# Kernel optimization log

Measured on AMD Instinct MI355X. Metric: run time of the kernel, lower is better.

## Reference

```python
import jax, jax.numpy as jnp
import numpy as np

H = 1024        # hidden_dim
NH = 8          # num_heads
HD = H // NH    # head_dim
EPS = 1e-5


def setup_inputs() -> dict:
    key = jax.random.key(0)
    ks = jax.random.split(key, 16)
    s = 0.02
    d = {
        'x': jax.random.normal(ks[0], (2, 2048, H), dtype=jnp.float32),
        'ln1_g': jnp.ones((H,), jnp.float32), 'ln1_b': jnp.zeros((H,), jnp.float32),
        'ln2_g': jnp.ones((H,), jnp.float32), 'ln2_b': jnp.zeros((H,), jnp.float32),
        'Wq': jax.random.normal(ks[1], (H, H), jnp.float32) * s,
        'bq': jnp.zeros((H,), jnp.float32),
        'Wk': jax.random.normal(ks[2], (H, H), jnp.float32) * s,
        'bk': jnp.zeros((H,), jnp.float32),
        'Wv': jax.random.normal(ks[3], (H, H), jnp.float32) * s,
        'bv': jnp.zeros((H,), jnp.float32),
        'Wo': jax.random.normal(ks[4], (H, H), jnp.float32) * s,
        'bo': jnp.zeros((H,), jnp.float32),
        'W1': jax.random.normal(ks[5], (H, 4 * H), jnp.float32) * s,
        'b1': jnp.zeros((4 * H,), jnp.float32),
        'W2': jax.random.normal(ks[6], (4 * H, H), jnp.float32) * s,
        'b2': jnp.zeros((H,), jnp.float32),
    }
    return d


def _layernorm(x, g, b):
    mu = jnp.mean(x, axis=-1, keepdims=True)
    var = jnp.mean(jnp.square(x - mu), axis=-1, keepdims=True)
    return (x - mu) * jax.lax.rsqrt(var + EPS) * g + b


def _block(x, ln1_g, ln1_b, ln2_g, ln2_b, Wq, bq, Wk, bk, Wv, bv, Wo, bo, W1, b1, W2, b2):
    B, S, _ = x.shape
    h = _layernorm(x, ln1_g, ln1_b)
    q = (h @ Wq + bq).reshape(B, S, NH, HD).transpose(0, 2, 1, 3)  # [B,NH,S,HD]
    k = (h @ Wk + bk).reshape(B, S, NH, HD).transpose(0, 2, 1, 3)
    v = (h @ Wv + bv).reshape(B, S, NH, HD).transpose(0, 2, 1, 3)
    scores = jnp.einsum('bhqd,bhkd->bhqk', q, k) / np.sqrt(HD)
    causal = jnp.tril(jnp.ones((S, S), bool))
    scores = jnp.where(causal, scores, -jnp.inf)
    attn = jax.nn.softmax(scores, axis=-1)
    y = jnp.einsum('bhqk,bhkd->bhqd', attn, v).transpose(0, 2, 1, 3).reshape(B, S, H)
    x = x + y @ Wo + bo
    h2 = _layernorm(x, ln2_g, ln2_b)
    m = jax.nn.gelu(h2 @ W1 + b1, approximate=False) @ W2 + b2
    return x + m


def reference(x, ln1_g, ln1_b, ln2_g, ln2_b, Wq, bq, Wk, bk, Wv, bv, Wo, bo, W1, b1, W2, b2):
    return _block(x, ln1_g, ln1_b, ln2_g, ln2_b, Wq, bq, Wk, bk, Wv, bv, Wo, bo, W1, b1, W2, b2)
```

## Files before the change

kernel.cpp:

```cpp
#include <hip/hip_runtime.h>
#include <hip/hip_bf16.h>
#include <math.h>

using bf16 = __hip_bfloat16;
typedef __attribute__((ext_vector_type(8))) short short8v;
typedef __attribute__((ext_vector_type(4))) float f32x4;

#define DEV __device__ __forceinline__

DEV void load_lds16(const bf16* gsrc, bf16* ldst) {
  __builtin_amdgcn_global_load_lds((const __attribute__((address_space(1))) void*)gsrc,
                                   (__attribute__((address_space(3))) void*)ldst, 16, 0, 0);
}

DEV void swz8(int& bx, int& by, int gx, int gy) {
  const int n = gx * gy, c = n >> 3;
  int lin = bx + gx * by;
  lin = (lin & 7) * c + (lin >> 3);
  bx = lin % gx; by = lin / gx;
}

DEV unsigned pack2bf(float a, float b) {
  bf16 ba = __float2bfloat16(a), bb = __float2bfloat16(b);
  return (unsigned)*(unsigned short*)&ba | ((unsigned)*(unsigned short*)&bb << 16);
}

__global__ __launch_bounds__(256) void prep_kernel(
    const float* __restrict__ Wq, const float* __restrict__ Wk, const float* __restrict__ Wv,
    const float* __restrict__ Wo, const float* __restrict__ W1, const float* __restrict__ W2,
    bf16* __restrict__ WqT, bf16* __restrict__ WkT, bf16* __restrict__ WvT,
    bf16* __restrict__ WoT, bf16* __restrict__ W1T, bf16* __restrict__ W2T,
    const float* __restrict__ x, const float* __restrict__ ln1g, const float* __restrict__ ln1b,
    bf16* __restrict__ h) {
  __shared__ float tile[64][65];
  const int b = blockIdx.x;
  if (b >= 3072) {
    const int row = b - 3072, t = threadIdx.x;
    const float4 v = ((const float4*)(x + (size_t)row * 1024))[t];
    float s = v.x + v.y + v.z + v.w;
#pragma unroll
    for (int mm = 1; mm < 64; mm <<= 1) s += __shfl_xor(s, mm);
    __shared__ float r1[4], r2[4];
    if ((t & 63) == 0) r1[t >> 6] = s;
    __syncthreads();
    const float mean = (r1[0] + r1[1] + r1[2] + r1[3]) * (1.0f / 1024.0f);
    const float d0 = v.x - mean, d1 = v.y - mean, d2 = v.z - mean, d3 = v.w - mean;
    float s2 = d0 * d0 + d1 * d1 + d2 * d2 + d3 * d3;
#pragma unroll
    for (int mm = 1; mm < 64; mm <<= 1) s2 += __shfl_xor(s2, mm);
    if ((t & 63) == 0) r2[t >> 6] = s2;
    __syncthreads();
    const float var = (r2[0] + r2[1] + r2[2] + r2[3]) * (1.0f / 1024.0f);
    const float rinv = rsqrtf(var + 1e-5f);
    const int c = t * 4;
    bf16* o = h + (size_t)row * 1024 + c;
    o[0] = __float2bfloat16(d0 * rinv * ln1g[c + 0] + ln1b[c + 0]);
    o[1] = __float2bfloat16(d1 * rinv * ln1g[c + 1] + ln1b[c + 1]);
    o[2] = __float2bfloat16(d2 * rinv * ln1g[c + 2] + ln1b[c + 2]);
    o[3] = __float2bfloat16(d3 * rinv * ln1g[c + 3] + ln1b[c + 3]);
    return;
  }
  const float* W; bf16* WT; int K, N, n0, k0;
  if (b < 1024) {
    const int which = b >> 8, t = b & 255;
    W  = (which == 0) ? Wq  : (which == 1) ? Wk  : (which == 2) ? Wv  : Wo;
    WT = (which == 0) ? WqT : (which == 1) ? WkT : (which == 2) ? WvT : WoT;
    K = 1024; N = 1024; n0 = (t & 15) * 64; k0 = (t >> 4) * 64;
  } else if (b < 2048) {
    const int t = b - 1024;
    W = W1; WT = W1T; K = 1024; N = 4096; n0 = (t & 63) * 64; k0 = (t >> 6) * 64;
  } else {
    const int t = b - 2048;
    W = W2; WT = W2T; K = 4096; N = 1024; n0 = (t & 15) * 64; k0 = (t >> 4) * 64;
  }
  const int tx = threadIdx.x & 15, ty = threadIdx.x >> 4;
#pragma unroll
  for (int p = 0; p < 4; ++p) {
    int r = p * 16 + ty;
    float4 vv = *(const float4*)&W[(size_t)(k0 + r) * N + n0 + tx * 4];
    tile[r][tx * 4 + 0] = vv.x; tile[r][tx * 4 + 1] = vv.y;
    tile[r][tx * 4 + 2] = vv.z; tile[r][tx * 4 + 3] = vv.w;
  }
  __syncthreads();
#pragma unroll
  for (int p = 0; p < 4; ++p) {
    int n = p * 16 + ty;
    bf16* dst = WT + (size_t)(n0 + n) * K + k0 + tx * 4;
#pragma unroll
    for (int j = 0; j < 4; ++j) dst[j] = __float2bfloat16(tile[tx * 4 + j][n]);
  }
}

__global__ __launch_bounds__(256) void ln_kernel(const float* __restrict__ x,
                                                 const float* __restrict__ g,
                                                 const float* __restrict__ b,
                                                 bf16* __restrict__ out) {
  const int row = blockIdx.x, t = threadIdx.x;
  const float4 v = ((const float4*)(x + (size_t)row * 1024))[t];
  float s = v.x + v.y + v.z + v.w;
#pragma unroll
  for (int mm = 1; mm < 64; mm <<= 1) s += __shfl_xor(s, mm);
  __shared__ float r1[4], r2[4];
  if ((t & 63) == 0) r1[t >> 6] = s;
  __syncthreads();
  const float mean = (r1[0] + r1[1] + r1[2] + r1[3]) * (1.0f / 1024.0f);
  const float d0 = v.x - mean, d1 = v.y - mean, d2 = v.z - mean, d3 = v.w - mean;
  float s2 = d0 * d0 + d1 * d1 + d2 * d2 + d3 * d3;
#pragma unroll
  for (int mm = 1; mm < 64; mm <<= 1) s2 += __shfl_xor(s2, mm);
  if ((t & 63) == 0) r2[t >> 6] = s2;
  __syncthreads();
  const float var = (r2[0] + r2[1] + r2[2] + r2[3]) * (1.0f / 1024.0f);
  const float rinv = rsqrtf(var + 1e-5f);
  const int c = t * 4;
  bf16* o = out + (size_t)row * 1024 + c;
  o[0] = __float2bfloat16(d0 * rinv * g[c + 0] + b[c + 0]);
  o[1] = __float2bfloat16(d1 * rinv * g[c + 1] + b[c + 1]);
  o[2] = __float2bfloat16(d2 * rinv * g[c + 2] + b[c + 2]);
  o[3] = __float2bfloat16(d3 * rinv * g[c + 3] + b[c + 3]);
}

template <int EPI>
__global__ __launch_bounds__(512, 2) void gemm256(
    const bf16* __restrict__ A, const bf16* __restrict__ BT,
    const float* __restrict__ bias0, const float* __restrict__ bias1, const float* __restrict__ bias2,
    void* __restrict__ outp, int M, int N, int K) {
  __shared__ bf16 As[4][256 * 32];
  __shared__ bf16 Bs[4][256 * 32];
  const int tid = threadIdx.x;
  const int w = tid >> 6, l = tid & 63;
  const int wm = w >> 2, wn = w & 3;
  const int c = l & 15, h4 = l >> 4;
  int bx = blockIdx.x, by = blockIdx.y;
  swz8(bx, by, gridDim.x, gridDim.y);
  const int m0 = by * 256, n0 = bx * 256;

  const float* bias;
  int zz = 0;
  if (EPI == 0) {
    zz = n0 >> 10;
    bias = ((zz == 0) ? bias0 : (zz == 1) ? bias1 : bias2) - (zz << 10);
  } else {
    bias = bias0;
  }

  const int rl = l >> 2;
  const int ch = (l & 3) * 8;
  const int nkt = K >> 5;

  f32x4 acc[8][4] = {};

  auto STAGE_A = [&](int t, int b) {
    const bf16* src = A + (size_t)(m0 + rl) * K + t * 32 + ch;
    load_lds16(src + (size_t)((w * 2 + 0) * 16) * K, &As[b][(w * 2 + 0) * 512]);
    load_lds16(src + (size_t)((w * 2 + 1) * 16) * K, &As[b][(w * 2 + 1) * 512]);
  };
  auto STAGE_B = [&](int t, int b) {
    const bf16* src = BT + (size_t)(n0 + rl) * K + t * 32 + ch;
    load_lds16(src + (size_t)((w * 2 + 0) * 16) * K, &Bs[b][(w * 2 + 0) * 512]);
    load_lds16(src + (size_t)((w * 2 + 1) * 16) * K, &Bs[b][(w * 2 + 1) * 512]);
  };

  STAGE_A(0, 0); STAGE_B(0, 0);
  STAGE_A(1, 1); STAGE_B(1, 1);
  STAGE_A(2, 2); STAGE_B(2, 2);
  asm volatile("s_waitcnt vmcnt(8)" ::: "memory");
  __builtin_amdgcn_sched_barrier(0);
  __builtin_amdgcn_s_barrier();

  for (int t = 0; t < nkt; ++t) {
    const bf16* Ab = &As[t & 3][0];
    const bf16* Bb = &Bs[t & 3][0];
    short8v a[4], b[4];
#pragma unroll
    for (int i = 0; i < 4; ++i)
      a[i] = *(const short8v*)&Ab[(wm * 128 + i * 16 + c) * 32 + h4 * 8];
#pragma unroll
    for (int i = 0; i < 4; ++i)
      b[i] = *(const short8v*)&Bb[(wn * 64 + i * 16 + c) * 32 + h4 * 8];
    if (t + 3 < nkt) STAGE_A(t + 3, (t + 3) & 3);
    asm volatile("s_waitcnt lgkmcnt(0)" ::: "memory");
    __builtin_amdgcn_sched_barrier(0);
    __builtin_amdgcn_s_setprio(1);
#pragma unroll
    for (int mi = 0; mi < 4; ++mi)
#pragma unroll
      for (int ni = 0; ni < 4; ++ni)
        acc[mi][ni] = __builtin_amdgcn_mfma_f32_16x16x32_bf16(a[mi], b[ni], acc[mi][ni], 0, 0, 0);
    __builtin_amdgcn_s_setprio(0);
#pragma unroll
    for (int i = 0; i < 4; ++i)
      a[i] = *(const short8v*)&Ab[(wm * 128 + 64 + i * 16 + c) * 32 + h4 * 8];
    if (t + 3 < nkt) STAGE_B(t + 3, (t + 3) & 3);
    asm volatile("s_waitcnt lgkmcnt(0)" ::: "memory");
    __builtin_amdgcn_sched_barrier(0);
    __builtin_amdgcn_s_setprio(1);
#pragma unroll
    for (int mi = 0; mi < 4; ++mi)
#pragma unroll
      for (int ni = 0; ni < 4; ++ni)
        acc[4 + mi][ni] = __builtin_amdgcn_mfma_f32_16x16x32_bf16(a[mi], b[ni], acc[4 + mi][ni], 0, 0, 0);
    __builtin_amdgcn_s_setprio(0);
    if (t < nkt - 3)       asm volatile("s_waitcnt vmcnt(8)" ::: "memory");
    else if (t == nkt - 3) asm volatile("s_waitcnt vmcnt(4)" ::: "memory");
    else                   asm volatile("s_waitcnt vmcnt(0)" ::: "memory");
    __builtin_amdgcn_sched_barrier(0);
    __builtin_amdgcn_s_barrier();
  }

#pragma unroll
  for (int mi = 0; mi < 8; ++mi) {
#pragma unroll
    for (int ni = 0; ni < 4; ++ni) {
#pragma unroll
      for (int r = 0; r < 4; ++r) {
        const int m = m0 + wm * 128 + mi * 16 + h4 * 4 + r;
        const int n = n0 + wn * 64 + ni * 16 + c;
        const float vv = acc[mi][ni][r] + bias[n];
        if (EPI == 0) {
          const int bb = m >> 11, ss = m & 2047;
          const int n1 = n - (zz << 10);
          const int hh = n1 >> 7, dd = n1 & 127;
          ((bf16*)outp)[(size_t)zz * 4194304 + (((size_t)bb * 8 + hh) * 2048 + ss) * 128 + dd] =
              __float2bfloat16(vv);
        } else {
          const size_t idx = (size_t)m * N + n;
          const float u = 0.7978845608028654f * (vv + 0.044715f * vv * vv * vv);
          const float tt = __expf(2.0f * u);
          const float th = 1.0f - 2.0f / (tt + 1.0f);
          ((bf16*)outp)[idx] = __float2bfloat16(0.5f * vv * (1.0f + th));
        }
      }
    }
  }
}

template <int EPI, int MI>
__global__ __launch_bounds__(256) void gemm128(
    const bf16* __restrict__ A, const bf16* __restrict__ BT,
    const float* __restrict__ bias0, const float* __restrict__ bias1, const float* __restrict__ bias2,
    const float* __restrict__ res, void* __restrict__ outp,
    int M, int N, int K) {
  __shared__ bf16 As[2][MI * 1024];
  __shared__ bf16 Bs[2][128 * 32];
  const int tid = threadIdx.x;
  const int w = tid >> 6, l = tid & 63;
  const int wr = w >> 1, wc = w & 1;
  const int col = l & 15, hi = l >> 4;
  int bx = blockIdx.x, by = blockIdx.y;
  swz8(bx, by, gridDim.x, gridDim.y);
  const int m0 = by * (32 * MI), n0 = bx * 128;

  const float* bias = bias0;

  const int srow = l >> 2;
  const int scol = ((l & 3) ^ ((l >> 4) & 3)) * 8;
  const int rs = col * 4 + (hi ^ ((l >> 2) & 3));
  f32x4 acc[MI][4] = {};

  const int nk = K >> 5;
#pragma unroll
  for (int j = 0; j < MI / 2; ++j) {
    const int grp = w * (MI / 2) + j;
    load_lds16(A + (size_t)(m0 + grp * 16 + srow) * K + scol, &As[0][grp * 512]);
  }
#pragma unroll
  for (int j = 0; j < 2; ++j) {
    const int grp = w * 2 + j;
    load_lds16(BT + (size_t)(n0 + grp * 16 + srow) * K + scol, &Bs[0][grp * 512]);
  }
  __syncthreads();

  int cur = 0;
  for (int kt = 0; kt < nk; ++kt) {
    if (kt + 1 < nk) {
      const int k0n = (kt + 1) * 32;
#pragma unroll
      for (int j = 0; j < MI / 2; ++j) {
        const int grp = w * (MI / 2) + j;
        load_lds16(A + (size_t)(m0 + grp * 16 + srow) * K + k0n + scol, &As[cur ^ 1][grp * 512]);
      }
#pragma unroll
      for (int j = 0; j < 2; ++j) {
        const int grp = w * 2 + j;
        load_lds16(BT + (size_t)(n0 + grp * 16 + srow) * K + k0n + scol, &Bs[cur ^ 1][grp * 512]);
      }
    }
    __builtin_amdgcn_sched_barrier(0);

    short8v af[MI], bfr[4];
#pragma unroll
    for (int i = 0; i < MI; ++i)
      af[i] = *(const short8v*)&As[cur][(wr * MI + i) * 512 + rs * 8];
#pragma unroll
    for (int i = 0; i < 4; ++i)
      bfr[i] = *(const short8v*)&Bs[cur][(wc * 4 + i) * 512 + rs * 8];
#pragma unroll
    for (int mi = 0; mi < MI; ++mi)
#pragma unroll
      for (int ni = 0; ni < 4; ++ni)
        acc[mi][ni] = __builtin_amdgcn_mfma_f32_16x16x32_bf16(af[mi], bfr[ni], acc[mi][ni], 0, 0, 0);
    __syncthreads();
    cur ^= 1;
  }

#pragma unroll
  for (int mi = 0; mi < MI; ++mi) {
#pragma unroll
    for (int ni = 0; ni < 4; ++ni) {
#pragma unroll
      for (int r = 0; r < 4; ++r) {
        const int m = m0 + wr * (16 * MI) + mi * 16 + hi * 4 + r;
        const int n = n0 + wc * 64 + ni * 16 + col;
        const float vv = acc[mi][ni][r] + bias[n];
        const size_t idx = (size_t)m * N + n;
        ((float*)outp)[idx] = res[idx] + vv;
      }
    }
  }
}

__global__ __launch_bounds__(512, 1) void gemm_sk2(
    const bf16* __restrict__ A, const bf16* __restrict__ BT,
    const float* __restrict__ bias, const float* __restrict__ res, float* __restrict__ outp,
    int M, int N, int K) {
  __shared__ __align__(16) char lds_raw[131072];
  const int tid = threadIdx.x;
  const int w = tid >> 6, l = tid & 63;
  const int grp = w >> 2, wg = w & 3;
  const int wr = wg >> 1, wc = wg & 1;
  const int col = l & 15, hi = l >> 4;
  int bx = blockIdx.x, by = blockIdx.y;
  swz8(bx, by, gridDim.x, gridDim.y);
  const int m0 = by * 128, n0 = bx * 128;

  const int rl = l >> 2;
  const int ch = (l & 3) * 8;
  f32x4 acc[4][4] = {};

  const int KH = K >> 1;
  const int kbase = grp * KH;
  const int nkt = KH >> 5;

  auto ABUF = [&](int b) { return (bf16*)(lds_raw + grp * 65536 + b * 16384); };
  auto BBUF = [&](int b) { return (bf16*)(lds_raw + grp * 65536 + b * 16384 + 8192); };

  auto STAGE = [&](int t, int b) {
    const bf16* srcA = A + (size_t)(m0 + rl) * K + kbase + t * 32 + ch;
    const bf16* srcB = BT + (size_t)(n0 + rl) * K + kbase + t * 32 + ch;
    bf16* Ab = ABUF(b); bf16* Bb = BBUF(b);
    load_lds16(srcA + (size_t)((wg * 2 + 0) * 16) * K, Ab + (wg * 2 + 0) * 512);
    load_lds16(srcA + (size_t)((wg * 2 + 1) * 16) * K, Ab + (wg * 2 + 1) * 512);
    load_lds16(srcB + (size_t)((wg * 2 + 0) * 16) * K, Bb + (wg * 2 + 0) * 512);
    load_lds16(srcB + (size_t)((wg * 2 + 1) * 16) * K, Bb + (wg * 2 + 1) * 512);
  };

  STAGE(0, 0); STAGE(1, 1); STAGE(2, 2);
  asm volatile("s_waitcnt vmcnt(8)" ::: "memory");
  __builtin_amdgcn_sched_barrier(0);
  __builtin_amdgcn_s_barrier();

  for (int t = 0; t < nkt; ++t) {
    const bf16* Ab = ABUF(t & 3);
    const bf16* Bb = BBUF(t & 3);
    short8v af[4], bf_[4];
#pragma unroll
    for (int i = 0; i < 4; ++i) {
      af[i]  = *(const short8v*)&Ab[(wr * 64 + i * 16 + col) * 32 + hi * 8];
      bf_[i] = *(const short8v*)&Bb[(wc * 64 + i * 16 + col) * 32 + hi * 8];
    }
    if (t + 3 < nkt) STAGE(t + 3, (t + 3) & 3);
    asm volatile("s_waitcnt lgkmcnt(0)" ::: "memory");
    __builtin_amdgcn_sched_barrier(0);
    __builtin_amdgcn_s_setprio(1);
#pragma unroll
    for (int mi = 0; mi < 4; ++mi)
#pragma unroll
      for (int ni = 0; ni < 4; ++ni)
        acc[mi][ni] = __builtin_amdgcn_mfma_f32_16x16x32_bf16(af[mi], bf_[ni], acc[mi][ni], 0, 0, 0);
    __builtin_amdgcn_s_setprio(0);
    if (t < nkt - 3)       asm volatile("s_waitcnt vmcnt(8)" ::: "memory");
    else if (t == nkt - 3) asm volatile("s_waitcnt vmcnt(4)" ::: "memory");
    else                   asm volatile("s_waitcnt vmcnt(0)" ::: "memory");
    __builtin_amdgcn_sched_barrier(0);
    __builtin_amdgcn_s_barrier();
  }

  float* dump = (float*)lds_raw;
  if (grp == 1) {
#pragma unroll
    for (int mi = 0; mi < 4; ++mi)
#pragma unroll
      for (int ni = 0; ni < 4; ++ni)
#pragma unroll
        for (int r = 0; r < 4; ++r)
          dump[(wr * 64 + mi * 16 + hi * 4 + r) * 130 + wc * 64 + ni * 16 + col] = acc[mi][ni][r];
  }
  __syncthreads();
  if (grp == 0) {
#pragma unroll
    for (int mi = 0; mi < 4; ++mi) {
#pragma unroll
      for (int ni = 0; ni < 4; ++ni) {
#pragma unroll
        for (int r = 0; r < 4; ++r) {
          const int lrow = wr * 64 + mi * 16 + hi * 4 + r;
          const int lcol = wc * 64 + ni * 16 + col;
          const int m = m0 + lrow, n = n0 + lcol;
          const size_t idx = (size_t)m * N + n;
          outp[idx] = res[idx] + acc[mi][ni][r] + dump[lrow * 130 + lcol] + bias[n];
        }
      }
    }
  }
}

__global__ __launch_bounds__(512) void attn_kernel(const bf16* __restrict__ q,
                                                   const bf16* __restrict__ k,
                                                   const bf16* __restrict__ v,
                                                   bf16* __restrict__ y) {
  __shared__ __align__(16) char lds_raw[157696];
  int p = blockIdx.x, bh = blockIdx.y;
  swz8(p, bh, 16, 16);
  const int tid = threadIdx.x;
  const int w = tid >> 6, l = tid & 63;
  const int grp = w >> 2, wg = w & 3;
  const int col = l & 15, hi = l >> 4;

  const bf16* kbase = k + (size_t)bh * 2048 * 128;
  const bf16* vbase = v + (size_t)bh * 2048 * 128;
  const int bb = bh >> 3, hh = bh & 7;

  bf16* Psw = (bf16*)(lds_raw + 139264 + (size_t)w * 2304);

  const int klr = (l >> 4);
  const int kblk0 = l & 15;
  const int vr = (l & 31) * 2;
  const int vcb = (wg * 2 + (l >> 5)) * 16;

  const float scale = 0.08838834764831845f;

  for (int half = 0; half < 2; ++half) {
    const int qt = half ? p : (31 - p);
    const int q0 = qt * 64;
    const int T = qt + 1;
    const int n0 = (T + 1) >> 1;
    const int myn = grp ? (T >> 1) : n0;
    const int tb = grp ? n0 : 0;

    short8v qf[4];
    const bf16* qp = q + ((size_t)bh * 2048 + q0 + wg * 16 + col) * 128;
#pragma unroll
    for (int c = 0; c < 4; ++c) qf[c] = *(const short8v*)(qp + c * 32 + hi * 8);

    f32x4 o[8] = {};
    float mx = -1e30f, sm = 0.f;

    if (myn > 0) {
      bf16* Ks0 = (bf16*)(lds_raw + (size_t)(grp * 2 + 0) * 16384);
      bf16* Vt0 = (bf16*)(lds_raw + 65536 + (size_t)(grp * 2 + 0) * 18432);
#pragma unroll
      for (int j = 0; j < 4; ++j) {
        const int lr = j * 4 + klr;
        const int blk = kblk0 ^ (lr & 7);
        load_lds16(kbase + (size_t)(tb * 64 + wg * 16 + lr) * 128 + blk * 8,
                   Ks0 + wg * 2048 + j * 512);
      }
      const bf16* vsrc = vbase + (size_t)(tb * 64 + vr) * 128 + vcb;
      short8v v00 = *(const short8v*)vsrc;
      short8v v01 = *(const short8v*)(vsrc + 8);
      short8v v10 = *(const short8v*)(vsrc + 128);
      short8v v11 = *(const short8v*)(vsrc + 136);
#pragma unroll
      for (int i = 0; i < 8; ++i) {
        *(unsigned int*)&Vt0[(vcb + i) * 72 + vr] =
            ((unsigned int)(unsigned short)v00[i]) | (((unsigned int)(unsigned short)v10[i]) << 16);
        *(unsigned int*)&Vt0[(vcb + 8 + i) * 72 + vr] =
            ((unsigned int)(unsigned short)v01[i]) | (((unsigned int)(unsigned short)v11[i]) << 16);
      }
    }
    __syncthreads();

    for (int it = 0; it < n0; ++it) {
      const int cur = it & 1;
      const bool active = it < myn;
      const bool havenext = (it + 1) < myn;
      bf16* KsCur = (bf16*)(lds_raw + (size_t)(grp * 2 + cur) * 16384);
      bf16* KsNxt = (bf16*)(lds_raw + (size_t)(grp * 2 + (cur ^ 1)) * 16384);
      bf16* VtCur = (bf16*)(lds_raw + 65536 + (size_t)(grp * 2 + cur) * 18432);
      bf16* VtNxt = (bf16*)(lds_raw + 65536 + (size_t)(grp * 2 + (cur ^ 1)) * 18432);

      short8v v00, v01, v10, v11;
      if (havenext) {
        const int nt = tb + it + 1;
#pragma unroll
        for (int j = 0; j < 4; ++j) {
          const int lr = j * 4 + klr;
          const int blk = kblk0 ^ (lr & 7);
          load_lds16(kbase + (size_t)(nt * 64 + wg * 16 + lr) * 128 + blk * 8,
                     KsNxt + wg * 2048 + j * 512);
        }
        const bf16* vsrc = vbase + (size_t)(nt * 64 + vr) * 128 + vcb;
        v00 = *(const short8v*)vsrc;
        v01 = *(const short8v*)(vsrc + 8);
        v10 = *(const short8v*)(vsrc + 128);
        v11 = *(const short8v*)(vsrc + 136);
      }

      if (active) {
        const int ktile = tb + it;
        f32x4 s[4] = {};
        __builtin_amdgcn_s_setprio(1);
#pragma unroll
        for (int c4 = 0; c4 < 4; ++c4) {
#pragma unroll
          for (int kg = 0; kg < 4; ++kg) {
            const int kr = kg * 16 + col;
            short8v kf = *(const short8v*)&KsCur[kr * 128 + ((c4 * 32 + hi * 8) ^ ((col & 7) << 3))];
            s[kg] = __builtin_amdgcn_mfma_f32_16x16x32_bf16(kf, qf[c4], s[kg], 0, 0, 0);
          }
        }
        __builtin_amdgcn_s_setprio(0);

        const bool diag = (ktile == qt);
        const int qloc = wg * 16 + col;
#pragma unroll
        for (int kg = 0; kg < 4; ++kg) {
#pragma unroll
          for (int r = 0; r < 4; ++r) {
            float a = s[kg][r] * scale;
            if (diag && (kg * 16 + hi * 4 + r > qloc)) a = -1e30f;
            s[kg][r] = a;
          }
        }
        f32x4 m4;
#pragma unroll
        for (int r = 0; r < 4; ++r)
          m4[r] = fmaxf(fmaxf(s[0][r], s[1][r]), fmaxf(s[2][r], s[3][r]));
        float t = fmaxf(fmaxf(m4[0], m4[1]), fmaxf(m4[2], m4[3]));
        t = fmaxf(t, __shfl_xor(t, 16));
        t = fmaxf(t, __shfl_xor(t, 32));
        const float mn = fmaxf(mx, t);
        const float aa = __expf(mx - mn);
        float ps = 0.f;
        unsigned pk0[4], pk1[4];
#pragma unroll
        for (int kg = 0; kg < 4; ++kg) {
          const float p0 = __expf(s[kg][0] - mn);
          const float p1 = __expf(s[kg][1] - mn);
          const float p2 = __expf(s[kg][2] - mn);
          const float p3 = __expf(s[kg][3] - mn);
          ps += (p0 + p1) + (p2 + p3);
          pk0[kg] = pack2bf(p0, p1);
          pk1[kg] = pack2bf(p2, p3);
        }
        ps += __shfl_xor(ps, 16);
        ps += __shfl_xor(ps, 32);
        sm = sm * aa + ps;
        mx = mn;
#pragma unroll
        for (int kg = 0; kg < 4; ++kg) {
          *(unsigned*)&Psw[col * 72 + kg * 16 + hi * 4]     = pk0[kg];
          *(unsigned*)&Psw[col * 72 + kg * 16 + hi * 4 + 2] = pk1[kg];
        }
#pragma unroll
        for (int db = 0; db < 8; ++db) {
          o[db][0] *= aa; o[db][1] *= aa; o[db][2] *= aa; o[db][3] *= aa;
        }
      }

      if (havenext) {
#pragma unroll
        for (int i = 0; i < 8; ++i) {
          *(unsigned int*)&VtNxt[(vcb + i) * 72 + vr] =
              ((unsigned int)(unsigned short)v00[i]) | (((unsigned int)(unsigned short)v10[i]) << 16);
          *(unsigned int*)&VtNxt[(vcb + 8 + i) * 72 + vr] =
              ((unsigned int)(unsigned short)v01[i]) | (((unsigned int)(unsigned short)v11[i]) << 16);
        }
      }

      if (active) {
        asm volatile("s_waitcnt lgkmcnt(0)" ::: "memory");
        __builtin_amdgcn_s_setprio(1);
#pragma unroll
        for (int ks = 0; ks < 2; ++ks) {
          short8v pf = *(const short8v*)&Psw[col * 72 + ks * 32 + hi * 8];
#pragma unroll
          for (int db = 0; db < 8; ++db) {
            short8v vf = *(const short8v*)&VtCur[(db * 16 + col) * 72 + ks * 32 + hi * 8];
            o[db] = __builtin_amdgcn_mfma_f32_16x16x32_bf16(vf, pf, o[db], 0, 0, 0);
          }
        }
        __builtin_amdgcn_s_setprio(0);
      }
      __syncthreads();
    }

    if (grp == 1) {
      float* Mo = (float*)(lds_raw + (size_t)wg * 8448);
      float* Ml = (float*)(lds_raw + 33792 + (size_t)wg * 128);
#pragma unroll
      for (int db = 0; db < 8; ++db)
        *(f32x4*)&Mo[col * 132 + db * 16 + hi * 4] = o[db];
      if (hi == 0) { Ml[col * 2] = mx; Ml[col * 2 + 1] = sm; }
    }
    __syncthreads();
    if (grp == 0) {
      const float* Mo = (const float*)(lds_raw + (size_t)wg * 8448);
      const float* Ml = (const float*)(lds_raw + 33792 + (size_t)wg * 128);
      const float m1 = Ml[col * 2], l1 = Ml[col * 2 + 1];
      const float M = fmaxf(mx, m1);
      const float a0 = __expf(mx - M);
      const float a1 = __expf(m1 - M);
      const float inv = 1.0f / (sm * a0 + l1 * a1);
      const int qg = q0 + wg * 16 + col;
      bf16* yrow = y + ((size_t)bb * 2048 + qg) * 1024 + hh * 128;
#pragma unroll
      for (int db = 0; db < 8; ++db) {
        f32x4 rd = *(const f32x4*)&Mo[col * 132 + db * 16 + hi * 4];
        const unsigned w0 = pack2bf((o[db][0] * a0 + rd[0] * a1) * inv,
                                    (o[db][1] * a0 + rd[1] * a1) * inv);
        const unsigned w1 = pack2bf((o[db][2] * a0 + rd[2] * a1) * inv,
                                    (o[db][3] * a0 + rd[3] * a1) * inv);
        uint2 pk; pk.x = w0; pk.y = w1;
        *(uint2*)(yrow + db * 16 + hi * 4) = pk;
      }
    }
    __syncthreads();
  }
}

extern "C" void kernel_launch(void* const* d_in, const int* in_sizes, int n_in,
                              void* d_out, int out_size, void* d_ws, size_t ws_size,
                              hipStream_t stream) {
  const float* x    = (const float*)d_in[0];
  const float* ln1g = (const float*)d_in[1];
  const float* ln1b = (const float*)d_in[2];
  const float* ln2g = (const float*)d_in[3];
  const float* ln2b = (const float*)d_in[4];
  const float* Wq   = (const float*)d_in[5];
  const float* bq   = (const float*)d_in[6];
  const float* Wk   = (const float*)d_in[7];
  const float* bk   = (const float*)d_in[8];
  const float* Wv   = (const float*)d_in[9];
  const float* bv   = (const float*)d_in[10];
  const float* Wo   = (const float*)d_in[11];
  const float* bo   = (const float*)d_in[12];
  const float* W1   = (const float*)d_in[13];
  const float* b1   = (const float*)d_in[14];
  const float* W2   = (const float*)d_in[15];
  const float* b2   = (const float*)d_in[16];
  float* out = (float*)d_out;
  char* ws = (char*)d_ws;
  const size_t MB = 1024 * 1024;

  bf16* WqT = (bf16*)(ws + 0 * MB);
  bf16* WkT = (bf16*)(ws + 2 * MB);
  bf16* WvT = (bf16*)(ws + 4 * MB);
  bf16* WoT = (bf16*)(ws + 6 * MB);
  bf16* W1T = (bf16*)(ws + 8 * MB);
  bf16* W2T = (bf16*)(ws + 16 * MB);
  bf16* h   = (bf16*)(ws + 24 * MB);
  bf16* qb  = (bf16*)(ws + 32 * MB);
  bf16* kb  = (bf16*)(ws + 40 * MB);
  bf16* vb  = (bf16*)(ws + 48 * MB);
  bf16* y   = (bf16*)(ws + 56 * MB);
  bf16* g   = (bf16*)(ws + 32 * MB);
  float* x1 = (float*)(ws + 64 * MB);
  bf16* h2  = h;

  prep_kernel<<<7168, 256, 0, stream>>>(Wq, Wk, Wv, Wo, W1, W2, WqT, WkT, WvT, WoT, W1T, W2T,
                                        x, ln1g, ln1b, h);

  gemm256<0><<<dim3(12, 16), 512, 0, stream>>>(h, WqT, bq, bk, bv, qb, 4096, 3072, 1024);

  attn_kernel<<<dim3(16, 16), 512, 0, stream>>>(qb, kb, vb, y);

  gemm128<1, 2><<<dim3(8, 64), 256, 0, stream>>>(y, WoT, bo, nullptr, nullptr, x, x1,
                                                 4096, 1024, 1024);

  ln_kernel<<<4096, 256, 0, stream>>>(x1, ln2g, ln2b, h2);

  gemm256<2><<<dim3(16, 16), 512, 0, stream>>>(h2, W1T, b1, nullptr, nullptr, g,
                                               4096, 4096, 1024);

  gemm_sk2<<<dim3(8, 32), 512, 0, stream>>>(g, W2T, b2, x1, out, 4096, 1024, 4096);
}
```

Baseline: 220.9 us.

## Fold softmax scale into Q projection, lazy rescale, reuse split-K GEMM for Wo

The 1/sqrt(HD) attention scale is now applied to Q in the QKV GEMM epilogue, so the per-score multiply in the attention loop goes away and causal masking runs only on diagonal tiles. The online softmax skips the running-max update and output rescale when every lane's new tile max stays within 8 of the current max, which saves exp and multiply work on most tiles. The Wo projection drops the 128-tile gemm128 kernel and uses the existing gemm_sk2 split-K kernel with residual add. The lazy max update lets exp values reach about e^8 before a rescale, which is fine for fp32 but could cost some bf16 precision in P.

```diff
diff --git a/kernel.cpp b/kernel.cpp
--- a/kernel.cpp
+++ b/kernel.cpp
@@ -216,8 +216,9 @@
       for (int r = 0; r < 4; ++r) {
         const int m = m0 + wm * 128 + mi * 16 + h4 * 4 + r;
         const int n = n0 + wn * 64 + ni * 16 + c;
-        const float vv = acc[mi][ni][r] + bias[n];
+        float vv = acc[mi][ni][r] + bias[n];
         if (EPI == 0) {
+          if (zz == 0) vv *= 0.08838834764831845f;
           const int bb = m >> 11, ss = m & 2047;
           const int n1 = n - (zz << 10);
           const int hh = n1 >> 7, dd = n1 & 127;
@@ -230,91 +231,6 @@
           const float th = 1.0f - 2.0f / (tt + 1.0f);
           ((bf16*)outp)[idx] = __float2bfloat16(0.5f * vv * (1.0f + th));
         }
-      }
-    }
-  }
-}
-
-template <int EPI, int MI>
-__global__ __launch_bounds__(256) void gemm128(
-    const bf16* __restrict__ A, const bf16* __restrict__ BT,
-    const float* __restrict__ bias0, const float* __restrict__ bias1, const float* __restrict__ bias2,
-    const float* __restrict__ res, void* __restrict__ outp,
-    int M, int N, int K) {
-  __shared__ bf16 As[2][MI * 1024];
-  __shared__ bf16 Bs[2][128 * 32];
-  const int tid = threadIdx.x;
-  const int w = tid >> 6, l = tid & 63;
-  const int wr = w >> 1, wc = w & 1;
-  const int col = l & 15, hi = l >> 4;
-  int bx = blockIdx.x, by = blockIdx.y;
-  swz8(bx, by, gridDim.x, gridDim.y);
-  const int m0 = by * (32 * MI), n0 = bx * 128;
-
-  const float* bias = bias0;
-
-  const int srow = l >> 2;
-  const int scol = ((l & 3) ^ ((l >> 4) & 3)) * 8;
-  const int rs = col * 4 + (hi ^ ((l >> 2) & 3));
-  f32x4 acc[MI][4] = {};
-
-  const int nk = K >> 5;
-#pragma unroll
-  for (int j = 0; j < MI / 2; ++j) {
-    const int grp = w * (MI / 2) + j;
-    load_lds16(A + (size_t)(m0 + grp * 16 + srow) * K + scol, &As[0][grp * 512]);
-  }
-#pragma unroll
-  for (int j = 0; j < 2; ++j) {
-    const int grp = w * 2 + j;
-    load_lds16(BT + (size_t)(n0 + grp * 16 + srow) * K + scol, &Bs[0][grp * 512]);
-  }
-  __syncthreads();
-
-  int cur = 0;
-  for (int kt = 0; kt < nk; ++kt) {
-    if (kt + 1 < nk) {
-      const int k0n = (kt + 1) * 32;
-#pragma unroll
-      for (int j = 0; j < MI / 2; ++j) {
-        const int grp = w * (MI / 2) + j;
-        load_lds16(A + (size_t)(m0 + grp * 16 + srow) * K + k0n + scol, &As[cur ^ 1][grp * 512]);
-      }
-#pragma unroll
-      for (int j = 0; j < 2; ++j) {
-        const int grp = w * 2 + j;
-        load_lds16(BT + (size_t)(n0 + grp * 16 + srow) * K + k0n + scol, &Bs[cur ^ 1][grp * 512]);
-      }
-    }
-    __builtin_amdgcn_sched_barrier(0);
-
-    short8v af[MI], bfr[4];
-#pragma unroll
-    for (int i = 0; i < MI; ++i)
-      af[i] = *(const short8v*)&As[cur][(wr * MI + i) * 512 + rs * 8];
-#pragma unroll
-    for (int i = 0; i < 4; ++i)
-      bfr[i] = *(const short8v*)&Bs[cur][(wc * 4 + i) * 512 + rs * 8];
-#pragma unroll
-    for (int mi = 0; mi < MI; ++mi)
-#pragma unroll
-      for (int ni = 0; ni < 4; ++ni)
-        acc[mi][ni] = __builtin_amdgcn_mfma_f32_16x16x32_bf16(af[mi], bfr[ni], acc[mi][ni], 0, 0, 0);
-    __syncthreads();
-    cur ^= 1;
-  }
-
-#pragma unroll
-  for (int mi = 0; mi < MI; ++mi) {
-#pragma unroll
-    for (int ni = 0; ni < 4; ++ni) {
-#pragma unroll
-      for (int r = 0; r < 4; ++r) {
-        const int m = m0 + wr * (16 * MI) + mi * 16 + hi * 4 + r;
-        const int n = n0 + wc * 64 + ni * 16 + col;
-        const float vv = acc[mi][ni][r] + bias[n];
-        const size_t idx = (size_t)m * N + n;
-        ((float*)outp)[idx] = res[idx] + vv;
       }
     }
   }
@@ -438,8 +354,6 @@
   const int vr = (l & 31) * 2;
   const int vcb = (wg * 2 + (l >> 5)) * 16;
 
-  const float scale = 0.08838834764831845f;
-
   for (int half = 0; half < 2; ++half) {
     const int qt = half ? p : (31 - p);
     const int q0 = qt * 64;
@@ -524,14 +438,12 @@
 
         const bool diag = (ktile == qt);
         const int qloc = wg * 16 + col;
-#pragma unroll
-        for (int kg = 0; kg < 4; ++kg) {
-#pragma unroll
-          for (int r = 0; r < 4; ++r) {
-            float a = s[kg][r] * scale;
-            if (diag && (kg * 16 + hi * 4 + r > qloc)) a = -1e30f;
-            s[kg][r] = a;
-          }
+        if (diag) {
+#pragma unroll
+          for (int kg = 0; kg < 4; ++kg)
+#pragma unroll
+            for (int r = 0; r < 4; ++r)
+              if (kg * 16 + hi * 4 + r > qloc) s[kg][r] = -1e30f;
         }
         f32x4 m4;
 #pragma unroll
@@ -540,8 +452,19 @@
         float t = fmaxf(fmaxf(m4[0], m4[1]), fmaxf(m4[2], m4[3]));
         t = fmaxf(t, __shfl_xor(t, 16));
         t = fmaxf(t, __shfl_xor(t, 32));
-        const float mn = fmaxf(mx, t);
-        const float aa = __expf(mx - mn);
+        float mn;
+        if (__all(t <= mx + 8.0f)) {
+          mn = mx;
+        } else {
+          mn = fmaxf(mx, t);
+          const float aa = __expf(mx - mn);
+          sm *= aa;
+#pragma unroll
+          for (int db = 0; db < 8; ++db) {
+            o[db][0] *= aa; o[db][1] *= aa; o[db][2] *= aa; o[db][3] *= aa;
+          }
+          mx = mn;
+        }
         float ps = 0.f;
         unsigned pk0[4], pk1[4];
 #pragma unroll
@@ -556,16 +479,11 @@
         }
         ps += __shfl_xor(ps, 16);
         ps += __shfl_xor(ps, 32);
-        sm = sm * aa + ps;
-        mx = mn;
+        sm += ps;
 #pragma unroll
         for (int kg = 0; kg < 4; ++kg) {
           *(unsigned*)&Psw[col * 72 + kg * 16 + hi * 4]     = pk0[kg];
           *(unsigned*)&Psw[col * 72 + kg * 16 + hi * 4 + 2] = pk1[kg];
-        }
-#pragma unroll
-        for (int db = 0; db < 8; ++db) {
-          o[db][0] *= aa; o[db][1] *= aa; o[db][2] *= aa; o[db][3] *= aa;
         }
       }
 
@@ -676,8 +594,7 @@
 
   attn_kernel<<<dim3(16, 16), 512, 0, stream>>>(qb, kb, vb, y);
 
-  gemm128<1, 2><<<dim3(8, 64), 256, 0, stream>>>(y, WoT, bo, nullptr, nullptr, x, x1,
-                                                 4096, 1024, 1024);
+  gemm_sk2<<<dim3(8, 32), 512, 0, stream>>>(y, WoT, bo, x, x1, 4096, 1024, 1024);
 
   ln_kernel<<<4096, 256, 0, stream>>>(x1, ln2g, ln2b, h2);
 
```

New measurement: 226.4 us. 2.5% more time.
